# Performance work log

Hardware: AMD Instinct MI355X
Metric: run time of the kernel (lower is better)

Reference implementation:

```python
import jax, jax.numpy as jnp
import numpy as np

B, S, HID = 2, 2048, 1024
NUM_HEADS, HEAD_DIM = 16, 64
GRID_SIZE = 16                 # crop_size // patch_size
ROT_DIM = 2 * (HEAD_DIM // 3 // 2)  # = 20, per axial segment (d, h, w)


def setup_inputs() -> dict:
    key = jax.random.key(0)
    ks = jax.random.split(key, 9)
    sc = 1.0 / np.sqrt(HID)
    return {
        "hidden_states": jax.random.normal(ks[0], (B, S, HID), jnp.float32),
        "Wq": jax.random.normal(ks[1], (HID, HID), jnp.float32) * sc,
        "bq": jax.random.normal(ks[2], (HID,), jnp.float32) * 0.02,
        "Wk": jax.random.normal(ks[3], (HID, HID), jnp.float32) * sc,
        "bk": jax.random.normal(ks[4], (HID,), jnp.float32) * 0.02,
        "Wv": jax.random.normal(ks[5], (HID, HID), jnp.float32) * sc,
        "bv": jax.random.normal(ks[6], (HID,), jnp.float32) * 0.02,
        "Wo": jax.random.normal(ks[7], (HID, HID), jnp.float32) * sc,
        "bo": jax.random.normal(ks[8], (HID,), jnp.float32) * 0.02,
    }


def _rotate(x, pos):
    # x: [B, H, S, D], pos: [S] int. Matches torch rotate_queries_or_keys:
    # sin/cos are TILED (repeat) along the last dim, not interleaved.
    D = x.shape[-1]
    half = D // 2
    omega = 1.0 / (10000.0 ** (jnp.arange(half, dtype=x.dtype) / half))
    freq = pos.astype(x.dtype)[:, None] * omega           # [S, half]
    sin = jnp.tile(jnp.sin(freq), (1, 2))                 # [S, D]
    cos = jnp.tile(jnp.cos(freq), (1, 2))
    y = x.reshape(x.shape[:-1] + (half, 2))
    rot = jnp.stack((-y[..., 1], y[..., 0]), axis=-1).reshape(x.shape)
    return x * cos + rot * sin


def _apply_axial_rope(qk, frame_ids, height_ids, width_ids):
    d = ROT_DIM
    parts = [
        _rotate(qk[..., 0:d], frame_ids),
        _rotate(qk[..., d:2 * d], height_ids),
        _rotate(qk[..., 2 * d:3 * d], width_ids),
    ]
    if 3 * d < qk.shape[-1]:
        parts.append(qk[..., 3 * d:])  # un-rotated tail
    return jnp.concatenate(parts, axis=-1)


def reference(hidden_states, Wq, bq, Wk, bk, Wv, bv, Wo, bo):
    Bq, Sq, _ = hidden_states.shape

    def heads(x):  # [B,S,HID] -> [B,H,S,Dh]
        return x.reshape(Bq, Sq, NUM_HEADS, HEAD_DIM).transpose(0, 2, 1, 3)

    q = heads(hidden_states @ Wq + bq)
    k = heads(hidden_states @ Wk + bk)
    v = heads(hidden_states @ Wv + bv)

    # 3D axial position ids from flat token index
    ids = jnp.arange(Sq)
    tokens_per_frame = GRID_SIZE * GRID_SIZE
    frame_ids = ids // tokens_per_frame
    rem = ids - tokens_per_frame * frame_ids
    height_ids = rem // GRID_SIZE
    width_ids = rem - GRID_SIZE * height_ids

    k = _apply_axial_rope(k, frame_ids, height_ids, width_ids)
    q = _apply_axial_rope(q, frame_ids, height_ids, width_ids)

    scaling = HEAD_DIM ** -0.5
    scores = jnp.einsum("bhqd,bhkd->bhqk", q, k) * scaling
    probs = jax.nn.softmax(scores.astype(jnp.float32), axis=-1).astype(q.dtype)
    ctx = jnp.einsum("bhqk,bhkd->bhqd", probs, v)
    ctx = ctx.transpose(0, 2, 1, 3).reshape(Bq, Sq, HID)
    return ctx @ Wo + bo
```

## Files before the change

### kernel.cpp

```cpp
#include <hip/hip_runtime.h>
#include <hip/hip_bf16.h>

#define B_   2
#define S_   2048
#define HID_ 1024
#define NH_  16
#define HD_  64

typedef __hip_bfloat16 bf16;
typedef __attribute__((ext_vector_type(8))) short s8v;
typedef __attribute__((ext_vector_type(4))) short s4v;
typedef __attribute__((ext_vector_type(4))) float f4v;

#define QSCALE 0.18033688011112042f

__device__ __forceinline__ unsigned short f2b_rne(float x) {
    unsigned int u = __float_as_uint(x);
    u += 0x7fffu + ((u >> 16) & 1u);
    return (unsigned short)(u >> 16);
}

__device__ __forceinline__ void gload_lds16(const void* g, void* l) {
    __builtin_amdgcn_global_load_lds(
        (const __attribute__((address_space(1))) void*)g,
        (__attribute__((address_space(3))) void*)l, 16, 0, 0);
}

__device__ __forceinline__ s4v pack_p(float p0, float p1, float p2, float p3) {
    union { uint2 u; s4v s; } c;
    c.u.x = __builtin_amdgcn_perm(__float_as_uint(p1), __float_as_uint(p0), 0x07060302u);
    c.u.y = __builtin_amdgcn_perm(__float_as_uint(p3), __float_as_uint(p2), 0x07060302u);
    return c.s;
}

__global__ __launch_bounds__(256) void prep_kernel(
    const float* __restrict__ X,
    const float* __restrict__ W0, const float* __restrict__ W1,
    const float* __restrict__ W2, const float* __restrict__ W3,
    unsigned short* __restrict__ Xb,
    unsigned short* __restrict__ T0, unsigned short* __restrict__ T1,
    unsigned short* __restrict__ T2, unsigned short* __restrict__ T3)
{
    const int z = blockIdx.z;
    const int t = threadIdx.x;

    if (z >= 4) {
        const size_t base = ((size_t)(z - 4) * 256 + blockIdx.y * 16 + blockIdx.x) * 4096;
        #pragma unroll
        for (int p = 0; p < 4; ++p) {
            const size_t i = base + p * 1024 + t * 4;
            const float4 f = *reinterpret_cast<const float4*>(X + i);
            ushort4 u;
            u.x = f2b_rne(f.x); u.y = f2b_rne(f.y); u.z = f2b_rne(f.z); u.w = f2b_rne(f.w);
            *reinterpret_cast<ushort4*>(Xb + i) = u;
        }
        return;
    }

    const float* __restrict__ W = (z == 0) ? W0 : (z == 1) ? W1 : (z == 2) ? W2 : W3;
    unsigned short* __restrict__ T = (z == 0) ? T0 : (z == 1) ? T1 : (z == 2) ? T2 : T3;

    __shared__ float Tl[64][65];
    const int n0 = blockIdx.x * 64, k0 = blockIdx.y * 64;
    const int rr = t >> 4, c4 = (t & 15) * 4;

    #pragma unroll
    for (int i = 0; i < 4; ++i) {
        const int kr = i * 16 + rr;
        const float4 f = *reinterpret_cast<const float4*>(W + (size_t)(k0 + kr) * HID_ + n0 + c4);
        Tl[c4 + 0][kr] = f.x; Tl[c4 + 1][kr] = f.y;
        Tl[c4 + 2][kr] = f.z; Tl[c4 + 3][kr] = f.w;
    }
    __syncthreads();
    #pragma unroll
    for (int i = 0; i < 4; ++i) {
        const int nr = i * 16 + rr;
        ushort4 u;
        u.x = f2b_rne(Tl[nr][c4 + 0]); u.y = f2b_rne(Tl[nr][c4 + 1]);
        u.z = f2b_rne(Tl[nr][c4 + 2]); u.w = f2b_rne(Tl[nr][c4 + 3]);
        *reinterpret_cast<ushort4*>(T + (size_t)(n0 + nr) * HID_ + k0 + c4) = u;
    }
}

__device__ __forceinline__ void mfma_mainloop(
    const unsigned short* __restrict__ Ag, const unsigned short* __restrict__ Bg,
    unsigned short* As, unsigned short* Bs,
    int m0, int n0, int t, f4v acc[4][4])
{
    const int w = t >> 6, lane = t & 63;
    const int l15 = lane & 15, qd = lane >> 4;
    const int wm = (w & 1) * 64, wn = (w >> 1) * 64;
    const int srow = w * 8 + (lane >> 3);
    const int lc8  = (((lane & 7) ^ (lane >> 3)) * 8);

    for (int k0 = 0; k0 < HID_; k0 += 64) {
        __syncthreads();
        #pragma unroll
        for (int it = 0; it < 4; ++it) {
            const int row = it * 32 + srow;
            const int sb = (it * 256 + w * 64) * 8;
            gload_lds16(Ag + (size_t)(m0 + row) * HID_ + k0 + lc8, As + sb);
            gload_lds16(Bg + (size_t)(n0 + row) * HID_ + k0 + lc8, Bs + sb);
        }
        __syncthreads();
        #pragma unroll
        for (int kc = 0; kc < 2; ++kc) {
            const int p = ((kc * 4 + qd) ^ (l15 & 7)) * 8;
            s8v af[4], bf[4];
            #pragma unroll
            for (int mt = 0; mt < 4; ++mt)
                af[mt] = *reinterpret_cast<const s8v*>(As + (wm + mt * 16 + l15) * 64 + p);
            #pragma unroll
            for (int nt = 0; nt < 4; ++nt)
                bf[nt] = *reinterpret_cast<const s8v*>(Bs + (wn + nt * 16 + l15) * 64 + p);
            #pragma unroll
            for (int mt = 0; mt < 4; ++mt)
                #pragma unroll
                for (int nt = 0; nt < 4; ++nt)
                    acc[mt][nt] = __builtin_amdgcn_mfma_f32_16x16x32_bf16(
                        af[mt], bf[nt], acc[mt][nt], 0, 0, 0);
        }
    }
}

__global__ __launch_bounds__(256) void gemm_qkv_kernel(
    const unsigned short* __restrict__ Xb,
    const unsigned short* __restrict__ Wqt, const unsigned short* __restrict__ Wkt,
    const unsigned short* __restrict__ Wvt,
    const float* __restrict__ bq, const float* __restrict__ bk, const float* __restrict__ bv,
    unsigned short* __restrict__ Qb, unsigned short* __restrict__ Kb,
    unsigned short* __restrict__ Vt)
{
    const int z = blockIdx.z;
    const unsigned short* __restrict__ Bt = (z == 0) ? Wqt : (z == 1) ? Wkt : Wvt;
    const float* __restrict__ bias = (z == 0) ? bq : (z == 1) ? bk : bv;

    const int n0 = blockIdx.x * 128, m0 = blockIdx.y * 128;
    const int t = threadIdx.x;
    const int w = t >> 6, lane = t & 63;
    const int l15 = lane & 15, qd = lane >> 4;
    const int wm = (w & 1) * 64, wn = (w >> 1) * 64;

    __shared__ unsigned short As[128 * 64];
    __shared__ unsigned short Bs[128 * 64];

    f4v acc[4][4];
    #pragma unroll
    for (int mt = 0; mt < 4; ++mt)
        #pragma unroll
        for (int nt = 0; nt < 4; ++nt) acc[mt][nt] = (f4v){0.f, 0.f, 0.f, 0.f};

    mfma_mainloop(Xb, Bt, As, Bs, m0, n0, t, acc);

    const float osc = (z == 0) ? QSCALE : 1.f;

    #pragma unroll
    for (int nt = 0; nt < 4; ++nt) {
        const int col = n0 + wn + nt * 16 + l15;
        const int h = col >> 6, d = col & 63;
        const float bsc = bias[col];
        const int seg = d / 20;
        const int ds  = d - seg * 20;
        const float om   = __expf(-0.9210340372f * (float)(ds % 10));
        const float sign = (d & 1) ? 1.f : -1.f;

        #pragma unroll
        for (int mt = 0; mt < 4; ++mt) {
            const int mbase = m0 + wm + mt * 16 + qd * 4;
            const int b = mbase >> 11;
            const int sbase = mbase & 2047;
            if (z == 2) {
                ushort4 u;
                unsigned short* up = (unsigned short*)&u;
                #pragma unroll
                for (int r = 0; r < 4; ++r) up[r] = f2b_rne(acc[mt][nt][r] + bsc);
                *reinterpret_cast<ushort4*>(
                    Vt + ((size_t)(b * NH_ + h) * HD_ + d) * S_ + sbase) = u;
            } else {
                unsigned short* __restrict__ dst = (z == 0 ? Qb : Kb)
                    + ((size_t)(b * NH_ + h) * S_ + sbase) * HD_ + d;
                #pragma unroll
                for (int r = 0; r < 4; ++r) {
                    const int s = sbase + r;
                    float v = acc[mt][nt][r] + bsc;
                    const float xp = __shfl_xor(v, 1);
                    if (d < 60) {
                        const int rem = s & 255;
                        const float pos = (float)(seg == 0 ? (s >> 8)
                                               : (seg == 1 ? (rem >> 4) : (rem & 15)));
                        const float a = pos * om;
                        float sn, cs;
                        __sincosf(a, &sn, &cs);
                        v = v * cs + sign * xp * sn;
                    }
                    dst[(size_t)r * HD_] = f2b_rne(v * osc);
                }
            }
        }
    }
}

__global__ __launch_bounds__(256) void gemm_out_kernel(
    const unsigned short* __restrict__ Cb, const unsigned short* __restrict__ Wot,
    const float* __restrict__ bo, float* __restrict__ out)
{
    const int n0 = blockIdx.x * 128, m0 = blockIdx.y * 128;
    const int t = threadIdx.x;
    const int w = t >> 6, lane = t & 63;
    const int l15 = lane & 15, qd = lane >> 4;
    const int wm = (w & 1) * 64, wn = (w >> 1) * 64;

    __shared__ unsigned short As[128 * 64];
    __shared__ unsigned short Bs[128 * 64];

    f4v acc[4][4];
    #pragma unroll
    for (int mt = 0; mt < 4; ++mt)
        #pragma unroll
        for (int nt = 0; nt < 4; ++nt) acc[mt][nt] = (f4v){0.f, 0.f, 0.f, 0.f};

    mfma_mainloop(Cb, Wot, As, Bs, m0, n0, t, acc);

    #pragma unroll
    for (int nt = 0; nt < 4; ++nt) {
        const int col = n0 + wn + nt * 16 + l15;
        const float bsc = bo[col];
        #pragma unroll
        for (int mt = 0; mt < 4; ++mt) {
            const int mbase = m0 + wm + mt * 16 + qd * 4;
            #pragma unroll
            for (int r = 0; r < 4; ++r)
                out[(size_t)(mbase + r) * HID_ + col] = acc[mt][nt][r] + bsc;
        }
    }
}

__global__ __launch_bounds__(256, 2) void attn_kernel(
    const bf16* __restrict__ Qb, const bf16* __restrict__ Kb,
    const bf16* __restrict__ Vt, unsigned short* __restrict__ Cb)
{
    const int q0 = blockIdx.x * 128;
    const int bh = blockIdx.y;
    const int b  = bh >> 4, h = bh & 15;
    const int t  = threadIdx.x;
    const int w  = t >> 6;
    const int lane = t & 63;
    const int l15 = lane & 15, qd = lane >> 4;

    __shared__ unsigned short Ks[2][128 * 64];
    __shared__ unsigned short Vs[2][64 * 128];

    s8v bq[2][2];
    #pragma unroll
    for (int g = 0; g < 2; ++g) {
        const bf16* Qrow = Qb + ((size_t)bh * S_ + q0 + w * 32 + g * 16 + l15) * HD_ + qd * 8;
        bq[g][0] = *reinterpret_cast<const s8v*>(Qrow);
        bq[g][1] = *reinterpret_cast<const s8v*>(Qrow + 32);
    }

    f4v oacc[2][4];
    f4v lones[2];
    #pragma unroll
    for (int g = 0; g < 2; ++g) {
        lones[g] = (f4v){0.f, 0.f, 0.f, 0.f};
        #pragma unroll
        for (int dt = 0; dt < 4; ++dt) oacc[g][dt] = (f4v){0.f, 0.f, 0.f, 0.f};
    }

    s4v vone;
    { union { uint2 u; s4v s; } c; c.u = make_uint2(0x3F803F80u, 0x3F803F80u); vone = c.s; }

    const bf16* __restrict__ Kg = Kb + (size_t)bh * S_ * HD_;
    const bf16* __restrict__ Vg = Vt + (size_t)bh * HD_ * S_;

    const int krow = lane >> 3;
    const int ksw  = ((lane & 7) ^ krow) * 8;
    const int vrow = lane >> 4;

    auto stage = [&](int tile, unsigned short* Kd, unsigned short* Vd) {
        const int k0 = tile * 128;
        #pragma unroll
        for (int it = 0; it < 4; ++it) {
            gload_lds16(Kg + (size_t)(k0 + w * 32 + it * 8 + krow) * HD_ + ksw,
                        Kd + (w * 32 + it * 8) * 64);
        }
        #pragma unroll
        for (int it = 0; it < 4; ++it) {
            const int r = w * 16 + it * 4 + vrow;
            const int sv = ((lane & 15) ^ (r & 15)) * 8;
            gload_lds16(Vg + (size_t)r * S_ + k0 + sv,
                        Vd + (w * 16 + it * 4) * 128);
        }
    };

    stage(0, Ks[0], Vs[0]);

    for (int tt = 0; tt < S_ / 128; ++tt) {
        __builtin_amdgcn_s_waitcnt(0x0f70);
        __builtin_amdgcn_s_barrier();
        if (tt < S_ / 128 - 1)
            stage(tt + 1, Ks[(tt + 1) & 1], Vs[(tt + 1) & 1]);

        const unsigned short* K_ = Ks[tt & 1];
        const unsigned short* V_ = Vs[tt & 1];

        #pragma unroll
        for (int nt = 0; nt < 8; ++nt) {
            const unsigned short* kr = K_ + (nt * 16 + l15) * 64;
            const s8v ak0 = *reinterpret_cast<const s8v*>(kr + ((qd ^ (l15 & 7)) * 8));
            const s8v ak1 = *reinterpret_cast<const s8v*>(kr + (((qd + 4) ^ (l15 & 7)) * 8));

            s4v bv[4];
            #pragma unroll
            for (int dt = 0; dt < 4; ++dt) {
                const int r = dt * 16 + l15;
                const int c = nt * 2 + (qd >> 1);
                bv[dt] = *reinterpret_cast<const s4v*>(
                    V_ + r * 128 + ((c ^ l15) & 15) * 8 + (qd & 1) * 4);
            }

            #pragma unroll
            for (int g = 0; g < 2; ++g) {
                f4v zz = (f4v){0.f, 0.f, 0.f, 0.f};
                zz = __builtin_amdgcn_mfma_f32_16x16x32_bf16(ak0, bq[g][0], zz, 0, 0, 0);
                zz = __builtin_amdgcn_mfma_f32_16x16x32_bf16(ak1, bq[g][1], zz, 0, 0, 0);
                const float p0 = __builtin_amdgcn_exp2f(zz[0]);
                const float p1 = __builtin_amdgcn_exp2f(zz[1]);
                const float p2 = __builtin_amdgcn_exp2f(zz[2]);
                const float p3 = __builtin_amdgcn_exp2f(zz[3]);
                const s4v pf = pack_p(p0, p1, p2, p3);
                #pragma unroll
                for (int dt = 0; dt < 4; ++dt)
                    oacc[g][dt] = __builtin_amdgcn_mfma_f32_16x16x16bf16_1k(
                        pf, bv[dt], oacc[g][dt], 0, 0, 0);
                lones[g] = __builtin_amdgcn_mfma_f32_16x16x16bf16_1k(
                    pf, vone, lones[g], 0, 0, 0);
            }
        }
    }

    #pragma unroll
    for (int g = 0; g < 2; ++g) {
        #pragma unroll
        for (int r = 0; r < 4; ++r) {
            const float inv = 1.0f / lones[g][r];
            const int s = q0 + w * 32 + g * 16 + qd * 4 + r;
            unsigned short* __restrict__ dst =
                Cb + ((size_t)(b * S_ + s)) * HID_ + h * HD_ + l15;
            #pragma unroll
            for (int dt = 0; dt < 4; ++dt)
                dst[dt * 16] = f2b_rne(oacc[g][dt][r] * inv);
        }
    }
}

extern "C" void kernel_launch(void* const* d_in, const int* in_sizes, int n_in,
                              void* d_out, int out_size, void* d_ws, size_t ws_size,
                              hipStream_t stream)
{
    const float* X  = (const float*)d_in[0];
    const float* Wq = (const float*)d_in[1];
    const float* bq = (const float*)d_in[2];
    const float* Wk = (const float*)d_in[3];
    const float* bk = (const float*)d_in[4];
    const float* Wv = (const float*)d_in[5];
    const float* bv = (const float*)d_in[6];
    const float* Wo = (const float*)d_in[7];
    const float* bo = (const float*)d_in[8];
    float* out = (float*)d_out;

    const size_t QKV = (size_t)B_ * NH_ * S_ * HD_;
    const size_t WSZ = (size_t)HID_ * HID_;
    unsigned short* Wot = (unsigned short*)d_ws;
    unsigned short* Xb  = Wot + WSZ;
    unsigned short* Wqt = Xb  + QKV;
    unsigned short* Wkt = Wqt + WSZ;
    unsigned short* Wvt = Wkt + WSZ;
    unsigned short* Qb  = Wvt + WSZ;
    unsigned short* Kb  = Qb + QKV;
    unsigned short* Vt  = Kb + QKV;
    unsigned short* Cb  = Vt + QKV;

    prep_kernel<<<dim3(16, 16, 8), 256, 0, stream>>>(
        X, Wq, Wk, Wv, Wo, Xb, Wqt, Wkt, Wvt, Wot);
    gemm_qkv_kernel<<<dim3(8, 32, 3), 256, 0, stream>>>(
        Xb, Wqt, Wkt, Wvt, bq, bk, bv, Qb, Kb, Vt);
    attn_kernel<<<dim3(S_ / 128, B_ * NH_), 256, 0, stream>>>(
        (const bf16*)Qb, (const bf16*)Kb, (const bf16*)Vt, Cb);
    gemm_out_kernel<<<dim3(8, 32), 256, 0, stream>>>(Cb, Wot, bo, out);
}
```

Baseline: 205.9 us.

## Double-buffer LDS tiles in GEMM mainloop to overlap global loads with MFMA

```diff
diff --git a/kernel.cpp b/kernel.cpp
--- a/kernel.cpp
+++ b/kernel.cpp
@@ -82,9 +82,23 @@
     }
 }
 
-__device__ __forceinline__ void mfma_mainloop(
+__device__ __forceinline__ void gemm_stage(
     const unsigned short* __restrict__ Ag, const unsigned short* __restrict__ Bg,
     unsigned short* As, unsigned short* Bs,
+    int m0, int n0, int k0, int w, int srow, int lc8)
+{
+    #pragma unroll
+    for (int it = 0; it < 4; ++it) {
+        const int row = it * 32 + srow;
+        const int sb = (it * 256 + w * 64) * 8;
+        gload_lds16(Ag + (size_t)(m0 + row) * HID_ + k0 + lc8, As + sb);
+        gload_lds16(Bg + (size_t)(n0 + row) * HID_ + k0 + lc8, Bs + sb);
+    }
+}
+
+__device__ __forceinline__ void mfma_mainloop_db(
+    const unsigned short* __restrict__ Ag, const unsigned short* __restrict__ Bg,
+    unsigned short (*As)[128 * 64], unsigned short (*Bs)[128 * 64],
     int m0, int n0, int t, f4v acc[4][4])
 {
     const int w = t >> 6, lane = t & 63;
@@ -93,26 +107,27 @@
     const int srow = w * 8 + (lane >> 3);
     const int lc8  = (((lane & 7) ^ (lane >> 3)) * 8);
 
-    for (int k0 = 0; k0 < HID_; k0 += 64) {
-        __syncthreads();
-        #pragma unroll
-        for (int it = 0; it < 4; ++it) {
-            const int row = it * 32 + srow;
-            const int sb = (it * 256 + w * 64) * 8;
-            gload_lds16(Ag + (size_t)(m0 + row) * HID_ + k0 + lc8, As + sb);
-            gload_lds16(Bg + (size_t)(n0 + row) * HID_ + k0 + lc8, Bs + sb);
-        }
-        __syncthreads();
+    gemm_stage(Ag, Bg, As[0], Bs[0], m0, n0, 0, w, srow, lc8);
+
+    for (int kt = 0; kt < HID_ / 64; ++kt) {
+        __builtin_amdgcn_s_waitcnt(0x0f70);
+        __builtin_amdgcn_s_barrier();
+        if (kt < HID_ / 64 - 1)
+            gemm_stage(Ag, Bg, As[(kt + 1) & 1], Bs[(kt + 1) & 1],
+                       m0, n0, (kt + 1) * 64, w, srow, lc8);
+
+        const unsigned short* Acur = As[kt & 1];
+        const unsigned short* Bcur = Bs[kt & 1];
         #pragma unroll
         for (int kc = 0; kc < 2; ++kc) {
             const int p = ((kc * 4 + qd) ^ (l15 & 7)) * 8;
             s8v af[4], bf[4];
             #pragma unroll
             for (int mt = 0; mt < 4; ++mt)
-                af[mt] = *reinterpret_cast<const s8v*>(As + (wm + mt * 16 + l15) * 64 + p);
+                af[mt] = *reinterpret_cast<const s8v*>(Acur + (wm + mt * 16 + l15) * 64 + p);
             #pragma unroll
             for (int nt = 0; nt < 4; ++nt)
-                bf[nt] = *reinterpret_cast<const s8v*>(Bs + (wn + nt * 16 + l15) * 64 + p);
+                bf[nt] = *reinterpret_cast<const s8v*>(Bcur + (wn + nt * 16 + l15) * 64 + p);
             #pragma unroll
             for (int mt = 0; mt < 4; ++mt)
                 #pragma unroll
@@ -123,26 +138,25 @@
     }
 }
 
-__global__ __launch_bounds__(256) void gemm_qkv_kernel(
-    const unsigned short* __restrict__ Xb,
-    const unsigned short* __restrict__ Wqt, const unsigned short* __restrict__ Wkt,
-    const unsigned short* __restrict__ Wvt,
+__global__ __launch_bounds__(256, 2) void gemm_qkv_kernel(
+    const unsigned short* __restrict__ Xb, const unsigned short* __restrict__ Wt,
     const float* __restrict__ bq, const float* __restrict__ bk, const float* __restrict__ bv,
     unsigned short* __restrict__ Qb, unsigned short* __restrict__ Kb,
     unsigned short* __restrict__ Vt)
 {
-    const int z = blockIdx.z;
-    const unsigned short* __restrict__ Bt = (z == 0) ? Wqt : (z == 1) ? Wkt : Wvt;
+    const int n0g = blockIdx.x * 128;
+    const int z   = n0g >> 10;
+    const int n0  = n0g & 1023;
+    const int m0  = blockIdx.y * 128;
     const float* __restrict__ bias = (z == 0) ? bq : (z == 1) ? bk : bv;
 
-    const int n0 = blockIdx.x * 128, m0 = blockIdx.y * 128;
     const int t = threadIdx.x;
     const int w = t >> 6, lane = t & 63;
     const int l15 = lane & 15, qd = lane >> 4;
     const int wm = (w & 1) * 64, wn = (w >> 1) * 64;
 
-    __shared__ unsigned short As[128 * 64];
-    __shared__ unsigned short Bs[128 * 64];
+    __shared__ unsigned short As[2][128 * 64];
+    __shared__ unsigned short Bs[2][128 * 64];
 
     f4v acc[4][4];
     #pragma unroll
@@ -150,7 +164,7 @@
         #pragma unroll
         for (int nt = 0; nt < 4; ++nt) acc[mt][nt] = (f4v){0.f, 0.f, 0.f, 0.f};
 
-    mfma_mainloop(Xb, Bt, As, Bs, m0, n0, t, acc);
+    mfma_mainloop_db(Xb, Wt, As, Bs, m0, n0g, t, acc);
 
     const float osc = (z == 0) ? QSCALE : 1.f;
 
@@ -200,7 +214,7 @@
     }
 }
 
-__global__ __launch_bounds__(256) void gemm_out_kernel(
+__global__ __launch_bounds__(256, 2) void gemm_out_kernel(
     const unsigned short* __restrict__ Cb, const unsigned short* __restrict__ Wot,
     const float* __restrict__ bo, float* __restrict__ out)
 {
@@ -210,8 +224,8 @@
     const int l15 = lane & 15, qd = lane >> 4;
     const int wm = (w & 1) * 64, wn = (w >> 1) * 64;
 
-    __shared__ unsigned short As[128 * 64];
-    __shared__ unsigned short Bs[128 * 64];
+    __shared__ unsigned short As[2][128 * 64];
+    __shared__ unsigned short Bs[2][128 * 64];
 
     f4v acc[4][4];
     #pragma unroll
@@ -219,7 +233,7 @@
         #pragma unroll
         for (int nt = 0; nt < 4; ++nt) acc[mt][nt] = (f4v){0.f, 0.f, 0.f, 0.f};
 
-    mfma_mainloop(Cb, Wot, As, Bs, m0, n0, t, acc);
+    mfma_mainloop_db(Cb, Wot, As, Bs, m0, n0, t, acc);
 
     #pragma unroll
     for (int nt = 0; nt < 4; ++nt) {
@@ -383,8 +397,8 @@
 
     prep_kernel<<<dim3(16, 16, 8), 256, 0, stream>>>(
         X, Wq, Wk, Wv, Wo, Xb, Wqt, Wkt, Wvt, Wot);
-    gemm_qkv_kernel<<<dim3(8, 32, 3), 256, 0, stream>>>(
-        Xb, Wqt, Wkt, Wvt, bq, bk, bv, Qb, Kb, Vt);
+    gemm_qkv_kernel<<<dim3(24, 32), 256, 0, stream>>>(
+        Xb, Wqt, bq, bk, bv, Qb, Kb, Vt);
     attn_kernel<<<dim3(S_ / 128, B_ * NH_), 256, 0, stream>>>(
         (const bf16*)Qb, (const bf16*)Kb, (const bf16*)Vt, Cb);
     gemm_out_kernel<<<dim3(8, 32), 256, 0, stream>>>(Cb, Wot, bo, out);
```

New measurement: 190.5 us. 1.08x faster.
